# Kernel tuning notes

Measured on AMD Instinct MI355X. Metric: run time of the kernel, lower is better.

## Reference

```python
import jax, jax.numpy as jnp
import numpy as np

B, S, DIM = 2, 2048, 2048
H, KVH, HD = 16, 4, 128
G = H // KVH  # GQA groups = 4
THETA = 10000.0


def setup_inputs() -> dict:
    key = jax.random.key(0)
    k0, k1, k2, k3, k4 = jax.random.split(key, 5)
    x = jax.random.normal(k0, (B, S, DIM), jnp.float32)
    # RoPE table: [max_seq_len, head_dim//2, 2] holding (cos, sin)
    inv_freq = 1.0 / (THETA ** (jnp.arange(0, HD, 2, dtype=jnp.float32) / HD))
    angles = jnp.outer(jnp.arange(S, dtype=jnp.float32), inv_freq)  # [S, HD//2]
    freqs_cis = jnp.stack([jnp.cos(angles), jnp.sin(angles)], axis=-1)
    sc = 0.02
    wq = jax.random.normal(k1, (H * HD, DIM), jnp.float32) * sc
    wk = jax.random.normal(k2, (KVH * HD, DIM), jnp.float32) * sc
    wv = jax.random.normal(k3, (KVH * HD, DIM), jnp.float32) * sc
    wo = jax.random.normal(k4, (DIM, H * HD), jnp.float32) * sc
    return {"x": x, "freqs_cis": freqs_cis, "wq": wq, "wk": wk, "wv": wv, "wo": wo}


def apply_rope(x, freqs_cis):
    # x: [B, S, h, HD]; freqs_cis: [max_S, HD//2, 2]
    s = x.shape[1]
    xr = x.astype(jnp.float32).reshape(*x.shape[:-1], -1, 2)  # [B,S,h,HD//2,2]
    cos = freqs_cis[:s, :, 0][None, :, None, :]  # [1,S,1,HD//2]
    sin = freqs_cis[:s, :, 1][None, :, None, :]
    x0, x1 = xr[..., 0], xr[..., 1]
    out = jnp.stack([x0 * cos - x1 * sin, x0 * sin + x1 * cos], axis=-1)
    return out.reshape(x.shape).astype(x.dtype)


def reference(x, freqs_cis, wq, wk, wv, wo):
    b, s, d = x.shape
    q = (x @ wq.T).reshape(b, s, H, HD)
    k = (x @ wk.T).reshape(b, s, KVH, HD)
    v = (x @ wv.T).reshape(b, s, KVH, HD)
    q = apply_rope(q, freqs_cis)
    k = apply_rope(k, freqs_cis)
    # GQA expand: repeat_interleave along head dim
    k = jnp.repeat(k, G, axis=2)  # [b,s,H,HD]
    v = jnp.repeat(v, G, axis=2)
    q = jnp.swapaxes(q, 1, 2)  # [b,H,s,HD]
    k = jnp.swapaxes(k, 1, 2)
    v = jnp.swapaxes(v, 1, 2)
    scale = 1.0 / jnp.sqrt(jnp.asarray(HD, dtype=q.dtype))
    scores = jnp.einsum('bhqd,bhkd->bhqk', q, k) * scale  # [b,H,s,s]
    causal = jnp.tril(jnp.ones((s, s), dtype=bool))
    scores = jnp.where(causal[None, None], scores, jnp.finfo(scores.dtype).min)
    probs = jax.nn.softmax(scores, axis=-1)
    attn = jnp.einsum('bhqk,bhkd->bhqd', probs, v)  # [b,H,s,HD]
    attn = jnp.swapaxes(attn, 1, 2).reshape(b, s, H * HD)
    return attn @ wo.T
```

## Files before the change

kernel.cpp:

```cpp
#include <hip/hip_runtime.h>
#include <stdint.h>

#define B_ 2
#define S_ 2048
#define DIM_ 2048
#define H_ 16
#define KVH_ 4
#define HD_ 128

typedef short short8 __attribute__((ext_vector_type(8)));
typedef float f4 __attribute__((ext_vector_type(4)));
typedef unsigned short u16;

#define KSCALE (0.08838834764831845f * 1.4426950408889634f)

__device__ __forceinline__ float bf2f(u16 u) {
    union { unsigned int i; float f; } c; c.i = ((unsigned int)u) << 16; return c.f;
}
__device__ __forceinline__ u16 f2bf(float f) {
    union { float f; unsigned int i; } c; c.f = f;
    return (u16)((c.i + 0x7fffu + ((c.i >> 16) & 1u)) >> 16);
}

#define GLDS16(gp, lp) \
    __builtin_amdgcn_global_load_lds((const __attribute__((address_space(1))) unsigned int*)(gp), \
                                     (__attribute__((address_space(3))) unsigned int*)(lp), 16, 0, 0)

__global__ void cast_all(const float* __restrict__ x,  const float* __restrict__ wq,
                         const float* __restrict__ wk, const float* __restrict__ wv,
                         const float* __restrict__ wo,
                         u16* __restrict__ xb, u16* __restrict__ wqkvb, u16* __restrict__ wob) {
    int i = blockIdx.x * 256 + threadIdx.x;
    const float4* src; ushort4* dst; int j;
    if (i < 2097152)      { src = (const float4*)x;  dst = (ushort4*)xb;                 j = i; }
    else if (i < 3145728) { src = (const float4*)wq; dst = (ushort4*)wqkvb;              j = i - 2097152; }
    else if (i < 3407872) { src = (const float4*)wk; dst = (ushort4*)wqkvb + 1048576;    j = i - 3145728; }
    else if (i < 3670016) { src = (const float4*)wv; dst = (ushort4*)wqkvb + 1310720;    j = i - 3407872; }
    else                  { src = (const float4*)wo; dst = (ushort4*)wob;                j = i - 3670016; }
    float4 v = src[j];
    ushort4 o;
    o.x = f2bf(v.x); o.y = f2bf(v.y); o.z = f2bf(v.z); o.w = f2bf(v.w);
    dst[j] = o;
}

template<bool OUT_BF16>
__global__ __launch_bounds__(256) void gemm_bt(const u16* __restrict__ A,
                                               const u16* __restrict__ W,
                                               void* __restrict__ Cout,
                                               int M, int N, int K) {
    __shared__ u16 As[128 * 32];
    __shared__ u16 Bs[128 * 32];
    int t = threadIdx.x, lane = t & 63, w = t >> 6;
    int quad = lane >> 4, l16 = lane & 15;
    int wm = w & 1, wn = w >> 1;
    size_t m0 = (size_t)blockIdx.y * 128, n0 = (size_t)blockIdx.x * 128;

    int c0 = w * 2;
    int ar = c0 * 16 + (lane >> 2);
    int ac = (lane & 3) * 8;
    const u16* Abase = A + (m0 + ar) * (size_t)K + ac;
    const u16* Bbase = W + (n0 + ar) * (size_t)K + ac;
    u16* Adst = As + c0 * 512;
    u16* Bdst = Bs + c0 * 512;

    f4 acc[4][4];
    #pragma unroll
    for (int i = 0; i < 4; i++)
        #pragma unroll
        for (int j = 0; j < 4; j++) acc[i][j] = (f4){0.f, 0.f, 0.f, 0.f};

    int nk = K >> 5;
    for (int kt = 0; kt < nk; kt++) {
        const u16* ga = Abase + kt * 32;
        const u16* gb = Bbase + kt * 32;
        GLDS16(ga, Adst);
        GLDS16(ga + 16 * (size_t)K, Adst + 512);
        GLDS16(gb, Bdst);
        GLDS16(gb + 16 * (size_t)K, Bdst + 512);
        __syncthreads();
        short8 a[4], b[4];
        #pragma unroll
        for (int i = 0; i < 4; i++) a[i] = *(const short8*)&As[(wm * 64 + i * 16 + l16) * 32 + quad * 8];
        #pragma unroll
        for (int j = 0; j < 4; j++) b[j] = *(const short8*)&Bs[(wn * 64 + j * 16 + l16) * 32 + quad * 8];
        #pragma unroll
        for (int i = 0; i < 4; i++)
            #pragma unroll
            for (int j = 0; j < 4; j++)
                acc[i][j] = __builtin_amdgcn_mfma_f32_16x16x32_bf16(a[i], b[j], acc[i][j], 0, 0, 0);
        __syncthreads();
    }
    #pragma unroll
    for (int i = 0; i < 4; i++) {
        size_t row = m0 + wm * 64 + i * 16 + quad * 4;
        #pragma unroll
        for (int j = 0; j < 4; j++) {
            size_t col = n0 + wn * 64 + j * 16 + l16;
            #pragma unroll
            for (int r = 0; r < 4; r++) {
                if (OUT_BF16) ((u16*)Cout)[(row + r) * N + col] = f2bf(acc[i][j][r]);
                else          ((float*)Cout)[(row + r) * N + col] = acc[i][j][r];
            }
        }
    }
}

__global__ void rope_q(u16* __restrict__ QKV, const float* __restrict__ freqs) {
    int pc = blockIdx.x * 256 + threadIdx.x;
    int row = blockIdx.y;
    int s = row & (S_ - 1);
    int hd2 = pc & 63;
    float2 cs = ((const float2*)freqs)[s * 64 + hd2];
    ushort2* pp = (ushort2*)(QKV + (size_t)row * 3072);
    ushort2 v = pp[pc];
    float x0 = bf2f(v.x), x1 = bf2f(v.y);
    ushort2 ov;
    ov.x = f2bf((x0 * cs.x - x1 * cs.y) * KSCALE);
    ov.y = f2bf((x0 * cs.y + x1 * cs.x) * KSCALE);
    pp[pc] = ov;
}

__global__ __launch_bounds__(256) void pack_k(const u16* __restrict__ QKV,
                                              const float* __restrict__ freqs,
                                              u16* __restrict__ Kp) {
    int gid = blockIdx.x * 256 + threadIdx.x;
    int lane = gid & 63;
    int fid = (gid >> 6) & 15;
    int kt = (gid >> 10) & 31;
    int bk = gid >> 15;
    int b = bk >> 2, kvh = bk & 3;
    int n = fid >> 2, c = fid & 3;
    int l16 = lane & 15, quad = lane >> 4;
    int s = kt * 64 + n * 16 + l16;
    const u16* src = QKV + (size_t)(b * 2048 + s) * 3072 + 2048 + kvh * 128 + c * 32 + quad * 8;
    short8 v = *(const short8*)src;
    short8 o;
    #pragma unroll
    for (int jp = 0; jp < 4; jp++) {
        int hd2 = c * 16 + quad * 4 + jp;
        float2 cw = ((const float2*)freqs)[s * 64 + hd2];
        float x0 = bf2f((u16)v[2 * jp]), x1 = bf2f((u16)v[2 * jp + 1]);
        o[2 * jp]     = (short)f2bf(x0 * cw.x - x1 * cw.y);
        o[2 * jp + 1] = (short)f2bf(x0 * cw.y + x1 * cw.x);
    }
    *(short8*)&Kp[(size_t)gid * 8] = o;
}

__global__ __launch_bounds__(256) void pack_v(const u16* __restrict__ QKV, u16* __restrict__ Vp) {
    __shared__ u16 L[64 * 136];
    int bid = blockIdx.x;
    int bk = bid & 7, kt = bid >> 3;
    int b = bk >> 2, kvh = bk & 3;
    int t = threadIdx.x;
    const u16* src = QKV + (size_t)(b * 2048 + kt * 64) * 3072 + 2560 + kvh * 128;
    #pragma unroll
    for (int it = 0; it < 4; it++) {
        int idx = t + it * 256;
        int r = idx >> 4, c = idx & 15;
        *(short8*)&L[r * 136 + c * 8] = *(const short8*)(src + (size_t)r * 3072 + c * 8);
    }
    __syncthreads();
    u16* dst = Vp + ((size_t)bk * 32 + kt) * 8192;
    #pragma unroll
    for (int it = 0; it < 4; it++) {
        int idx = t + it * 256;
        int fid = idx >> 6, lane = idx & 63;
        int nt = fid >> 1, kc = fid & 1;
        int l16 = lane & 15, quad = lane >> 4;
        int hd = nt * 16 + l16;
        int s0 = kc * 32 + quad * 8;
        short8 v;
        #pragma unroll
        for (int j = 0; j < 8; j++) v[j] = (short)L[(s0 + j) * 136 + hd];
        *(short8*)&dst[(size_t)idx * 8] = v;
    }
}

__global__ __launch_bounds__(256) __attribute__((amdgpu_waves_per_eu(2, 2)))
void attn_kernel(const u16* __restrict__ QKV,
                 const u16* __restrict__ Kp,
                 const u16* __restrict__ Vp,
                 u16* __restrict__ Ob) {
    __shared__ u16 Ks[16 * 512];
    __shared__ u16 Vs[16 * 512];
    __shared__ u16 Ps[4 * 1024];
    int bid = blockIdx.x;
    int bk = bid & 7, pr = bid >> 3;
    int b = bk >> 2, kvh = bk & 3;
    int t = threadIdx.x, lane = t & 63, w = t >> 6, quad = lane >> 4, l16 = lane & 15;
    int l7 = l16 & 7, hi = l16 >> 3;
    int h = kvh * 4 + w;

    short8 ones;
    #pragma unroll
    for (int j = 0; j < 8; j++) ones[j] = (short)0x3F80;

    const u16* Kpb = Kp + (size_t)bk * 32 * 8192;
    const u16* Vpb = Vp + (size_t)bk * 32 * 8192;
    u16* P = Ps + w * 1024;

    for (int ph = 0; ph < 2; ph++) {
        int qt = ph ? pr : 127 - pr;
        int nkt = (qt >> 2) + 1;

        short8 qf[4];
        {
            const u16* qp = QKV + ((size_t)(b * S_ + qt * 16 + l16)) * 3072 + h * HD_ + quad * 8;
            #pragma unroll
            for (int c = 0; c < 4; c++) qf[c] = *(const short8*)(qp + c * 32);
        }
        float m_i = -3e38f;
        f4 ls = (f4){0.f, 0.f, 0.f, 0.f};
        f4 o[8];
        #pragma unroll
        for (int n = 0; n < 8; n++) o[n] = (f4){0.f, 0.f, 0.f, 0.f};

        for (int kt = 0; kt < nkt; kt++) {
            {
                const u16* ks = Kpb + (size_t)kt * 8192 + (w * 4) * 512 + lane * 8;
                const u16* vs = Vpb + (size_t)kt * 8192 + (w * 4) * 512 + lane * 8;
                #pragma unroll
                for (int i = 0; i < 4; i++) {
                    GLDS16(ks + i * 512, &Ks[(w * 4 + i) * 512]);
                    GLDS16(vs + i * 512, &Vs[(w * 4 + i) * 512]);
                }
            }
            __syncthreads();

            f4 sc[4];
            #pragma unroll
            for (int n = 0; n < 4; n++) sc[n] = (f4){0.f, 0.f, 0.f, 0.f};
            #pragma unroll
            for (int n = 0; n < 4; n++) {
                #pragma unroll
                for (int c = 0; c < 4; c++) {
                    short8 kf = *(const short8*)&Ks[(n * 4 + c) * 512 + lane * 8];
                    sc[n] = __builtin_amdgcn_mfma_f32_16x16x32_bf16(qf[c], kf, sc[n], 0, 0, 0);
                }
            }
            if (kt == nkt - 1) {
                int qrow0 = qt * 16 + quad * 4;
                #pragma unroll
                for (int n = 0; n < 4; n++) {
                    int colg = kt * 64 + n * 16 + l16;
                    #pragma unroll
                    for (int r = 0; r < 4; r++)
                        sc[n][r] = (colg <= qrow0 + r) ? sc[n][r] : -3e38f;
                }
            }
            float gm = fmaxf(fmaxf(sc[0][0], sc[0][1]), fmaxf(sc[0][2], sc[0][3]));
            #pragma unroll
            for (int n = 1; n < 4; n++)
                gm = fmaxf(gm, fmaxf(fmaxf(sc[n][0], sc[n][1]), fmaxf(sc[n][2], sc[n][3])));
            #pragma unroll
            for (int off = 1; off < 64; off <<= 1) gm = fmaxf(gm, __shfl_xor(gm, off, 64));
            float mnew = fmaxf(m_i, gm);
            if (mnew > m_i) {
                float al = exp2f(m_i - mnew);
                m_i = mnew;
                #pragma unroll
                for (int r = 0; r < 4; r++) ls[r] *= al;
                #pragma unroll
                for (int nt = 0; nt < 8; nt++)
                    #pragma unroll
                    for (int r = 0; r < 4; r++) o[nt][r] *= al;
            }
            #pragma unroll
            for (int n = 0; n < 4; n++) {
                #pragma unroll
                for (int r = 0; r < 4; r++) {
                    float p = exp2f(sc[n][r] - m_i);
                    union { float f; unsigned int u; } cv; cv.f = p;
                    int row = quad * 4 + r;
                    int sw = (n * 2 + hi) ^ (row & 7);
                    P[row * 64 + sw * 8 + l7] = (u16)(cv.u >> 16);
                }
            }
            __asm__ volatile("s_waitcnt lgkmcnt(0)" ::: "memory");

            #pragma unroll
            for (int kc = 0; kc < 2; kc++) {
                short8 af = *(const short8*)&P[l16 * 64 + (((kc * 4 + quad) ^ l7) << 3)];
                ls = __builtin_amdgcn_mfma_f32_16x16x32_bf16(af, ones, ls, 0, 0, 0);
                #pragma unroll
                for (int nt = 0; nt < 8; nt++) {
                    short8 vf = *(const short8*)&Vs[(nt * 2 + kc) * 512 + lane * 8];
                    o[nt] = __builtin_amdgcn_mfma_f32_16x16x32_bf16(af, vf, o[nt], 0, 0, 0);
                }
            }
            __syncthreads();
        }
        float rl[4];
        #pragma unroll
        for (int r = 0; r < 4; r++) rl[r] = 1.0f / ls[r];
        #pragma unroll
        for (int nt = 0; nt < 8; nt++)
            #pragma unroll
            for (int r = 0; r < 4; r++) {
                size_t row = (size_t)b * S_ + qt * 16 + quad * 4 + r;
                Ob[row * 2048 + h * HD_ + nt * 16 + l16] = f2bf(o[nt][r] * rl[r]);
            }
    }
}

extern "C" void kernel_launch(void* const* d_in, const int* in_sizes, int n_in,
                              void* d_out, int out_size, void* d_ws, size_t ws_size,
                              hipStream_t stream) {
    const float* x     = (const float*)d_in[0];
    const float* freqs = (const float*)d_in[1];
    const float* wq    = (const float*)d_in[2];
    const float* wk    = (const float*)d_in[3];
    const float* wv    = (const float*)d_in[4];
    const float* wo    = (const float*)d_in[5];
    float* out = (float*)d_out;

    char* p = (char*)d_ws;
    u16* xb    = (u16*)p; p += (size_t)4096 * 2048 * 2;
    u16* wqkvb = (u16*)p; p += (size_t)3072 * 2048 * 2;
    u16* wob   = (u16*)p; p += (size_t)2048 * 2048 * 2;
    u16* QKVb  = (u16*)p; p += (size_t)4096 * 3072 * 2;
    u16* Kpb   = (u16*)p; p += (size_t)8 * 32 * 8192 * 2;
    u16* Vpb   = (u16*)p; p += (size_t)8 * 32 * 8192 * 2;
    u16* attnb = xb;

    cast_all<<<18432, 256, 0, stream>>>(x, wq, wk, wv, wo, xb, wqkvb, wob);

    gemm_bt<true><<<dim3(24, 32), 256, 0, stream>>>(xb, wqkvb, QKVb, 4096, 3072, 2048);

    rope_q<<<dim3(4, 4096), 256, 0, stream>>>(QKVb, freqs);

    pack_k<<<1024, 256, 0, stream>>>(QKVb, freqs, Kpb);
    pack_v<<<256, 256, 0, stream>>>(QKVb, Vpb);

    attn_kernel<<<512, 256, 0, stream>>>(QKVb, Kpb, Vpb, attnb);

    gemm_bt<false><<<dim3(16, 32), 256, 0, stream>>>(attnb, wob, out, 4096, 2048, 2048);
}
```

Before: 324.0 us.

## Fuse RoPE and K/V packing into QKV GEMM epilogue; restructure attention grid

The QKV projection GEMM now applies RoPE and the softmax scale to Q in its epilogue. It also writes K and V straight into the packed MFMA-fragment layouts, which removes the separate rope_q, pack_k and pack_v kernels and their extra global memory round trips. The attention kernel no longer runs two phases per block. Each block now pairs a long and a short query tile across its waves (two heads × two query tiles), doubles the grid to 1024 blocks and raises waves_per_eu to 4. In exchange, the epilogue writes are scattered 2-byte stores that may coalesce poorly, and the short-tile waves sit idle through the extra K/V iterations.

```diff
diff --git a/kernel.cpp b/kernel.cpp
--- a/kernel.cpp
+++ b/kernel.cpp
@@ -105,79 +105,120 @@
     }
 }
 
-__global__ void rope_q(u16* __restrict__ QKV, const float* __restrict__ freqs) {
-    int pc = blockIdx.x * 256 + threadIdx.x;
-    int row = blockIdx.y;
-    int s = row & (S_ - 1);
-    int hd2 = pc & 63;
-    float2 cs = ((const float2*)freqs)[s * 64 + hd2];
-    ushort2* pp = (ushort2*)(QKV + (size_t)row * 3072);
-    ushort2 v = pp[pc];
-    float x0 = bf2f(v.x), x1 = bf2f(v.y);
-    ushort2 ov;
-    ov.x = f2bf((x0 * cs.x - x1 * cs.y) * KSCALE);
-    ov.y = f2bf((x0 * cs.y + x1 * cs.x) * KSCALE);
-    pp[pc] = ov;
-}
-
-__global__ __launch_bounds__(256) void pack_k(const u16* __restrict__ QKV,
-                                              const float* __restrict__ freqs,
-                                              u16* __restrict__ Kp) {
-    int gid = blockIdx.x * 256 + threadIdx.x;
-    int lane = gid & 63;
-    int fid = (gid >> 6) & 15;
-    int kt = (gid >> 10) & 31;
-    int bk = gid >> 15;
-    int b = bk >> 2, kvh = bk & 3;
-    int n = fid >> 2, c = fid & 3;
-    int l16 = lane & 15, quad = lane >> 4;
-    int s = kt * 64 + n * 16 + l16;
-    const u16* src = QKV + (size_t)(b * 2048 + s) * 3072 + 2048 + kvh * 128 + c * 32 + quad * 8;
-    short8 v = *(const short8*)src;
-    short8 o;
-    #pragma unroll
-    for (int jp = 0; jp < 4; jp++) {
-        int hd2 = c * 16 + quad * 4 + jp;
-        float2 cw = ((const float2*)freqs)[s * 64 + hd2];
-        float x0 = bf2f((u16)v[2 * jp]), x1 = bf2f((u16)v[2 * jp + 1]);
-        o[2 * jp]     = (short)f2bf(x0 * cw.x - x1 * cw.y);
-        o[2 * jp + 1] = (short)f2bf(x0 * cw.y + x1 * cw.x);
-    }
-    *(short8*)&Kp[(size_t)gid * 8] = o;
-}
-
-__global__ __launch_bounds__(256) void pack_v(const u16* __restrict__ QKV, u16* __restrict__ Vp) {
-    __shared__ u16 L[64 * 136];
-    int bid = blockIdx.x;
-    int bk = bid & 7, kt = bid >> 3;
-    int b = bk >> 2, kvh = bk & 3;
-    int t = threadIdx.x;
-    const u16* src = QKV + (size_t)(b * 2048 + kt * 64) * 3072 + 2560 + kvh * 128;
-    #pragma unroll
-    for (int it = 0; it < 4; it++) {
-        int idx = t + it * 256;
-        int r = idx >> 4, c = idx & 15;
-        *(short8*)&L[r * 136 + c * 8] = *(const short8*)(src + (size_t)r * 3072 + c * 8);
-    }
-    __syncthreads();
-    u16* dst = Vp + ((size_t)bk * 32 + kt) * 8192;
-    #pragma unroll
-    for (int it = 0; it < 4; it++) {
-        int idx = t + it * 256;
-        int fid = idx >> 6, lane = idx & 63;
-        int nt = fid >> 1, kc = fid & 1;
-        int l16 = lane & 15, quad = lane >> 4;
-        int hd = nt * 16 + l16;
-        int s0 = kc * 32 + quad * 8;
-        short8 v;
-        #pragma unroll
-        for (int j = 0; j < 8; j++) v[j] = (short)L[(s0 + j) * 136 + hd];
-        *(short8*)&dst[(size_t)idx * 8] = v;
-    }
-}
-
-__global__ __launch_bounds__(256) __attribute__((amdgpu_waves_per_eu(2, 2)))
-void attn_kernel(const u16* __restrict__ QKV,
+__global__ __launch_bounds__(256) void gemm_qkv(const u16* __restrict__ A,
+                                                const u16* __restrict__ W,
+                                                const float* __restrict__ freqs,
+                                                u16* __restrict__ Qb,
+                                                u16* __restrict__ Kp,
+                                                u16* __restrict__ Vp) {
+    __shared__ u16 As[128 * 32];
+    __shared__ u16 Bs[128 * 32];
+    const int K = 2048;
+    int t = threadIdx.x, lane = t & 63, w = t >> 6;
+    int quad = lane >> 4, l16 = lane & 15;
+    int wm = w & 1, wn = w >> 1;
+    int bx = blockIdx.x;
+    size_t m0 = (size_t)blockIdx.y * 128, n0 = (size_t)bx * 128;
+
+    int c0 = w * 2;
+    int ar = c0 * 16 + (lane >> 2);
+    int ac = (lane & 3) * 8;
+    const u16* Abase = A + (m0 + ar) * (size_t)K + ac;
+    const u16* Bbase = W + (n0 + ar) * (size_t)K + ac;
+    u16* Adst = As + c0 * 512;
+    u16* Bdst = Bs + c0 * 512;
+
+    f4 acc[4][4];
+    #pragma unroll
+    for (int i = 0; i < 4; i++)
+        #pragma unroll
+        for (int j = 0; j < 4; j++) acc[i][j] = (f4){0.f, 0.f, 0.f, 0.f};
+
+    for (int kt = 0; kt < 64; kt++) {
+        const u16* ga = Abase + kt * 32;
+        const u16* gb = Bbase + kt * 32;
+        GLDS16(ga, Adst);
+        GLDS16(ga + 16 * (size_t)K, Adst + 512);
+        GLDS16(gb, Bdst);
+        GLDS16(gb + 16 * (size_t)K, Bdst + 512);
+        __syncthreads();
+        short8 a[4], b[4];
+        #pragma unroll
+        for (int i = 0; i < 4; i++) a[i] = *(const short8*)&As[(wm * 64 + i * 16 + l16) * 32 + quad * 8];
+        #pragma unroll
+        for (int j = 0; j < 4; j++) b[j] = *(const short8*)&Bs[(wn * 64 + j * 16 + l16) * 32 + quad * 8];
+        #pragma unroll
+        for (int i = 0; i < 4; i++)
+            #pragma unroll
+            for (int j = 0; j < 4; j++)
+                acc[i][j] = __builtin_amdgcn_mfma_f32_16x16x32_bf16(a[i], b[j], acc[i][j], 0, 0, 0);
+        __syncthreads();
+    }
+
+    const float2* fr2 = (const float2*)freqs;
+    if (bx < 16) {
+        #pragma unroll
+        for (int i = 0; i < 4; i++) {
+            #pragma unroll
+            for (int j = 0; j < 4; j++) {
+                #pragma unroll
+                for (int r = 0; r < 4; r++) {
+                    int row = (int)m0 + wm * 64 + i * 16 + quad * 4 + r;
+                    int col = (int)n0 + wn * 64 + j * 16 + l16;
+                    float v = acc[i][j][r];
+                    float pv = __shfl_xor(v, 1, 64);
+                    int s = row & 2047;
+                    float2 cs = fr2[s * 64 + ((col & 127) >> 1)];
+                    float rot = (l16 & 1) ? (pv * cs.y + v * cs.x) : (v * cs.x - pv * cs.y);
+                    Qb[(size_t)row * 2048 + col] = f2bf(rot * KSCALE);
+                }
+            }
+        }
+    } else if (bx < 20) {
+        int kvh = bx - 16;
+        #pragma unroll
+        for (int i = 0; i < 4; i++) {
+            #pragma unroll
+            for (int j = 0; j < 4; j++) {
+                #pragma unroll
+                for (int r = 0; r < 4; r++) {
+                    int row = (int)m0 + wm * 64 + i * 16 + quad * 4 + r;
+                    int hd = wn * 64 + j * 16 + l16;
+                    float v = acc[i][j][r];
+                    float pv = __shfl_xor(v, 1, 64);
+                    int s = row & 2047, bb = row >> 11;
+                    float2 cs = fr2[s * 64 + (hd >> 1)];
+                    float rot = (l16 & 1) ? (pv * cs.y + v * cs.x) : (v * cs.x - pv * cs.y);
+                    int bk2 = bb * 4 + kvh, kt2 = s >> 6, s6 = s & 63;
+                    int idx = (((bk2 * 32 + kt2) * 16) + ((s6 >> 4) * 4 + (hd >> 5))) * 512
+                              + (((hd >> 3) & 3) * 16 + (s6 & 15)) * 8 + (hd & 7);
+                    Kp[idx] = f2bf(rot);
+                }
+            }
+        }
+    } else {
+        int kvh = bx - 20;
+        #pragma unroll
+        for (int i = 0; i < 4; i++) {
+            #pragma unroll
+            for (int j = 0; j < 4; j++) {
+                #pragma unroll
+                for (int r = 0; r < 4; r++) {
+                    int row = (int)m0 + wm * 64 + i * 16 + quad * 4 + r;
+                    int hd = wn * 64 + j * 16 + l16;
+                    int s = row & 2047, bb = row >> 11;
+                    int bk2 = bb * 4 + kvh, kt2 = s >> 6, s6 = s & 63;
+                    int idx = (((bk2 * 32 + kt2) * 16) + ((hd >> 4) * 2 + (s6 >> 5))) * 512
+                              + (((s6 >> 3) & 3) * 16 + (hd & 15)) * 8 + (s6 & 7);
+                    Vp[idx] = f2bf(acc[i][j][r]);
+                }
+            }
+        }
+    }
+}
+
+__global__ __launch_bounds__(256) __attribute__((amdgpu_waves_per_eu(4, 4)))
+void attn_kernel(const u16* __restrict__ Qb,
                  const u16* __restrict__ Kp,
                  const u16* __restrict__ Vp,
                  u16* __restrict__ Ob) {
@@ -185,48 +226,48 @@
     __shared__ u16 Vs[16 * 512];
     __shared__ u16 Ps[4 * 1024];
     int bid = blockIdx.x;
-    int bk = bid & 7, pr = bid >> 3;
+    int bk = bid & 7, pr = (bid >> 3) & 63, half = bid >> 9;
     int b = bk >> 2, kvh = bk & 3;
     int t = threadIdx.x, lane = t & 63, w = t >> 6, quad = lane >> 4, l16 = lane & 15;
     int l7 = l16 & 7, hi = l16 >> 3;
-    int h = kvh * 4 + w;
+    int h = kvh * 4 + half * 2 + (w & 1);
+    int qt = (w < 2) ? (127 - pr) : pr;
+    int nkt = (qt >> 2) + 1;
+    int nktL = 32 - (pr >> 2);
 
     short8 ones;
     #pragma unroll
     for (int j = 0; j < 8; j++) ones[j] = (short)0x3F80;
+
+    short8 qf[4];
+    {
+        const u16* qp = Qb + ((size_t)(b * S_ + qt * 16 + l16)) * 2048 + h * HD_ + quad * 8;
+        #pragma unroll
+        for (int c = 0; c < 4; c++) qf[c] = *(const short8*)(qp + c * 32);
+    }
+    float m_i = -3e38f;
+    f4 ls = (f4){0.f, 0.f, 0.f, 0.f};
+    f4 o[8];
+    #pragma unroll
+    for (int n = 0; n < 8; n++) o[n] = (f4){0.f, 0.f, 0.f, 0.f};
 
     const u16* Kpb = Kp + (size_t)bk * 32 * 8192;
     const u16* Vpb = Vp + (size_t)bk * 32 * 8192;
     u16* P = Ps + w * 1024;
 
-    for (int ph = 0; ph < 2; ph++) {
-        int qt = ph ? pr : 127 - pr;
-        int nkt = (qt >> 2) + 1;
-
-        short8 qf[4];
+    for (int kt = 0; kt < nktL; kt++) {
         {
-            const u16* qp = QKV + ((size_t)(b * S_ + qt * 16 + l16)) * 3072 + h * HD_ + quad * 8;
-            #pragma unroll
-            for (int c = 0; c < 4; c++) qf[c] = *(const short8*)(qp + c * 32);
-        }
-        float m_i = -3e38f;
-        f4 ls = (f4){0.f, 0.f, 0.f, 0.f};
-        f4 o[8];
-        #pragma unroll
-        for (int n = 0; n < 8; n++) o[n] = (f4){0.f, 0.f, 0.f, 0.f};
-
-        for (int kt = 0; kt < nkt; kt++) {
-            {
-                const u16* ks = Kpb + (size_t)kt * 8192 + (w * 4) * 512 + lane * 8;
-                const u16* vs = Vpb + (size_t)kt * 8192 + (w * 4) * 512 + lane * 8;
-                #pragma unroll
-                for (int i = 0; i < 4; i++) {
-                    GLDS16(ks + i * 512, &Ks[(w * 4 + i) * 512]);
-                    GLDS16(vs + i * 512, &Vs[(w * 4 + i) * 512]);
-                }
-            }
-            __syncthreads();
-
+            const u16* ks = Kpb + (size_t)kt * 8192 + (w * 4) * 512 + lane * 8;
+            const u16* vs = Vpb + (size_t)kt * 8192 + (w * 4) * 512 + lane * 8;
+            #pragma unroll
+            for (int i = 0; i < 4; i++) {
+                GLDS16(ks + i * 512, &Ks[(w * 4 + i) * 512]);
+                GLDS16(vs + i * 512, &Vs[(w * 4 + i) * 512]);
+            }
+        }
+        __syncthreads();
+
+        if (kt < nkt) {
             f4 sc[4];
             #pragma unroll
             for (int n = 0; n < 4; n++) sc[n] = (f4){0.f, 0.f, 0.f, 0.f};
@@ -288,19 +329,19 @@
                     o[nt] = __builtin_amdgcn_mfma_f32_16x16x32_bf16(af, vf, o[nt], 0, 0, 0);
                 }
             }
-            __syncthreads();
-        }
-        float rl[4];
-        #pragma unroll
-        for (int r = 0; r < 4; r++) rl[r] = 1.0f / ls[r];
-        #pragma unroll
-        for (int nt = 0; nt < 8; nt++)
-            #pragma unroll
-            for (int r = 0; r < 4; r++) {
-                size_t row = (size_t)b * S_ + qt * 16 + quad * 4 + r;
-                Ob[row * 2048 + h * HD_ + nt * 16 + l16] = f2bf(o[nt][r] * rl[r]);
-            }
-    }
+        }
+        __syncthreads();
+    }
+    float rl[4];
+    #pragma unroll
+    for (int r = 0; r < 4; r++) rl[r] = 1.0f / ls[r];
+    #pragma unroll
+    for (int nt = 0; nt < 8; nt++)
+        #pragma unroll
+        for (int r = 0; r < 4; r++) {
+            size_t row = (size_t)b * S_ + qt * 16 + quad * 4 + r;
+            Ob[row * 2048 + h * HD_ + nt * 16 + l16] = f2bf(o[nt][r] * rl[r]);
+        }
 }
 
 extern "C" void kernel_launch(void* const* d_in, const int* in_sizes, int n_in,
@@ -318,21 +359,16 @@
     u16* xb    = (u16*)p; p += (size_t)4096 * 2048 * 2;
     u16* wqkvb = (u16*)p; p += (size_t)3072 * 2048 * 2;
     u16* wob   = (u16*)p; p += (size_t)2048 * 2048 * 2;
-    u16* QKVb  = (u16*)p; p += (size_t)4096 * 3072 * 2;
+    u16* Qb    = (u16*)p; p += (size_t)4096 * 2048 * 2;
     u16* Kpb   = (u16*)p; p += (size_t)8 * 32 * 8192 * 2;
     u16* Vpb   = (u16*)p; p += (size_t)8 * 32 * 8192 * 2;
     u16* attnb = xb;
 
     cast_all<<<18432, 256, 0, stream>>>(x, wq, wk, wv, wo, xb, wqkvb, wob);
 
-    gemm_bt<true><<<dim3(24, 32), 256, 0, stream>>>(xb, wqkvb, QKVb, 4096, 3072, 2048);
-
-    rope_q<<<dim3(4, 4096), 256, 0, stream>>>(QKVb, freqs);
-
-    pack_k<<<1024, 256, 0, stream>>>(QKVb, freqs, Kpb);
-    pack_v<<<256, 256, 0, stream>>>(QKVb, Vpb);
-
-    attn_kernel<<<512, 256, 0, stream>>>(QKVb, Kpb, Vpb, attnb);
+    gemm_qkv<<<dim3(24, 32), 256, 0, stream>>>(xb, wqkvb, freqs, Qb, Kpb, Vpb);
+
+    attn_kernel<<<1024, 256, 0, stream>>>(Qb, Kpb, Vpb, attnb);
 
     gemm_bt<false><<<dim3(16, 32), 256, 0, stream>>>(attnb, wob, out, 4096, 2048, 2048);
 }
```

New measurement: 348.3 us. +7.5%, slower.
